# Optimization experiments

Hardware: AMD Instinct MI355X
Metric: run time of the kernel (lower is better)

The kernel has to match this reference:

```python
import jax, jax.numpy as jnp
import numpy as np

GAMMA = 0.99  # init kwarg


def _discounted_returns(ep_rs):
    # reversed running_add = running_add*gamma + r, emitted per step
    def step(carry, r):
        carry = carry * GAMMA + r
        return carry, carry
    _, out = jax.lax.scan(step, jnp.float32(0.0), ep_rs, reverse=True)
    return out  # [T]


def setup_inputs() -> dict:
    key = jax.random.key(0)
    k1, k2, k3 = jax.random.split(key, 3)
    T, A = 2097152, 18
    weight = jax.random.normal(k1, (T, A), dtype=jnp.float32)
    ep_rs = jax.random.normal(k2, (T,), dtype=jnp.float32)
    ep_as = jax.random.randint(k3, (T,), 0, A, dtype=jnp.int64)
    return {"weight": weight, "ep_rs": ep_rs, "ep_as": ep_as}


def reference(weight, ep_rs, ep_as):
    d = _discounted_returns(ep_rs)
    d = d - jnp.mean(d)
    # cross_entropy with reduction='none': -log_softmax(weight)[t, ep_as[t]]
    logp = jax.nn.log_softmax(weight, axis=-1)  # [T, A]
    neg_log_prob = -jnp.take_along_axis(logp, ep_as[:, None], axis=-1)[:, 0]  # [T]
    return jnp.mean(neg_log_prob * d)
```

## Files before the change

kernel.cpp:

```cpp
#include <hip/hip_runtime.h>
#include <math.h>

#define T_TOTAL 2097152
#define A_DIM   18
#define GAMMA_D 0.99

#define CHUNK 256
#define NC    (T_TOTAL / CHUNK)
#define KTR   14

#define ROWS_PER_TILE 256
#define NTILES  (T_TOTAL / ROWS_PER_TILE)
#define NB_MAIN 2048

__global__ void k_local(const float* __restrict__ r, double* __restrict__ L) {
    int c = blockIdx.x * blockDim.x + threadIdx.x;
    const float4* r4 = (const float4*)(r + (size_t)c * CHUNK);
    const double g  = GAMMA_D;
    const double g4 = g * g * g * g;
    double a0 = 0.0, a1 = 0.0, a2 = 0.0, a3 = 0.0;
    for (int k = CHUNK / 4 - 1; k >= 0; --k) {
        float4 v = r4[k];
        a0 = a0 * g4 + (double)v.x;
        a1 = a1 * g4 + (double)v.y;
        a2 = a2 * g4 + (double)v.z;
        a3 = a3 * g4 + (double)v.w;
    }
    L[c] = a0 + g * (a1 + g * (a2 + g * a3));
}

__global__ void k_carry(const double* __restrict__ L, double* __restrict__ carry,
                        double G) {
    int c = blockIdx.x * blockDim.x + threadIdx.x;
    double acc = 0.0;
    double w = 1.0;
    for (int m = 0; m < KTR; ++m) {
        int idx = c + 1 + m;
        if (idx < NC) acc += w * L[idx];
        w *= G;
    }
    carry[c] = acc;
}

__global__ void k_expand(const float* __restrict__ r,
                         const double* __restrict__ carry,
                         float* __restrict__ d) {
    int c = blockIdx.x * blockDim.x + threadIdx.x;
    const float4* r4 = (const float4*)(r + (size_t)c * CHUNK);
    float4*       d4 = (float4*)(d + (size_t)c * CHUNK);
    const double g = GAMMA_D;
    double cur = carry[c];
    for (int k = CHUNK / 4 - 1; k >= 0; --k) {
        float4 v = r4[k];
        double e3 = cur * g + (double)v.w;
        double e2 = e3 * g + (double)v.z;
        double e1 = e2 * g + (double)v.y;
        double e0 = e1 * g + (double)v.x;
        d4[k] = make_float4((float)e0, (float)e1, (float)e2, (float)e3);
        cur = e0;
    }
}

__launch_bounds__(256)
__global__ void k_main(const float* __restrict__ w, const int* __restrict__ act,
                       const float* __restrict__ d, double* __restrict__ partials) {
    __shared__ float  lds[ROWS_PER_TILE * A_DIM];
    __shared__ double red[12];
    const int tid = threadIdx.x;
    double s_d = 0.0, s_n = 0.0, s_nd = 0.0;

    for (int tile = blockIdx.x; tile < NTILES; tile += gridDim.x) {
        const float4* src = (const float4*)(w + (size_t)tile * ROWS_PER_TILE * A_DIM);
        float4* dst = (float4*)lds;
        __syncthreads();
        for (int idx = tid; idx < ROWS_PER_TILE * A_DIM / 4; idx += 256)
            dst[idx] = src[idx];
        __syncthreads();

        const int row = tile * ROWS_PER_TILE + tid;
        const float* wr = lds + tid * A_DIM;
        float m = wr[0];
        #pragma unroll
        for (int j = 1; j < A_DIM; ++j) m = fmaxf(m, wr[j]);
        float s = 0.0f;
        #pragma unroll
        for (int j = 0; j < A_DIM; ++j) s += expf(wr[j] - m);
        float lse  = m + logf(s);
        float nlp  = lse - wr[act[row]];
        float dv   = d[row];
        s_d  += (double)dv;
        s_n  += (double)nlp;
        s_nd += (double)nlp * (double)dv;
    }

    for (int off = 32; off > 0; off >>= 1) {
        s_d  += __shfl_down(s_d,  off, 64);
        s_n  += __shfl_down(s_n,  off, 64);
        s_nd += __shfl_down(s_nd, off, 64);
    }
    const int lane = tid & 63, wv = tid >> 6;
    if (lane == 0) { red[wv*3+0] = s_d; red[wv*3+1] = s_n; red[wv*3+2] = s_nd; }
    __syncthreads();
    if (tid == 0) {
        double a = 0.0, b = 0.0, c = 0.0;
        for (int i = 0; i < 4; ++i) { a += red[i*3]; b += red[i*3+1]; c += red[i*3+2]; }
        partials[blockIdx.x*3+0] = a;
        partials[blockIdx.x*3+1] = b;
        partials[blockIdx.x*3+2] = c;
    }
}

__global__ void k_final(const double* __restrict__ partials, float* __restrict__ out) {
    __shared__ double red[12];
    const int tid = threadIdx.x;
    double a = 0.0, b = 0.0, c = 0.0;
    for (int i = tid; i < NB_MAIN; i += 256) {
        a += partials[i*3+0];
        b += partials[i*3+1];
        c += partials[i*3+2];
    }
    for (int off = 32; off > 0; off >>= 1) {
        a += __shfl_down(a, off, 64);
        b += __shfl_down(b, off, 64);
        c += __shfl_down(c, off, 64);
    }
    const int lane = tid & 63, wv = tid >> 6;
    if (lane == 0) { red[wv*3+0] = a; red[wv*3+1] = b; red[wv*3+2] = c; }
    __syncthreads();
    if (tid == 0) {
        double A_ = 0.0, B_ = 0.0, C_ = 0.0;
        for (int i = 0; i < 4; ++i) { A_ += red[i*3]; B_ += red[i*3+1]; C_ += red[i*3+2]; }
        const double invT = 1.0 / (double)T_TOTAL;
        double res = (C_ - (A_ * invT) * B_) * invT;
        out[0] = (float)res;
    }
}

extern "C" void kernel_launch(void* const* d_in, const int* in_sizes, int n_in,
                              void* d_out, int out_size, void* d_ws, size_t ws_size,
                              hipStream_t stream) {
    const float* weight = (const float*)d_in[0];
    const float* ep_rs  = (const float*)d_in[1];
    const int*   ep_as  = (const int*)  d_in[2];
    float* out = (float*)d_out;

    char* ws = (char*)d_ws;
    double* L        = (double*)(ws);
    double* carry    = (double*)(ws + (1  << 16));
    double* partials = (double*)(ws + (2  << 16));
    float*  d        = (float*) (ws + (3  << 16));

    const double G = pow(GAMMA_D, (double)CHUNK);

    k_local <<<NC / 256, 256, 0, stream>>>(ep_rs, L);
    k_carry <<<NC / 256, 256, 0, stream>>>(L, carry, G);
    k_expand<<<NC / 256, 256, 0, stream>>>(ep_rs, carry, d);
    k_main  <<<NB_MAIN,  256, 0, stream>>>(weight, ep_as, d, partials);
    k_final <<<1,        256, 0, stream>>>(partials, out);
}
```

Baseline: 265.9 us.

## Fuse discounted-return expansion into main kernel via in-block weighted scan

Removes the k_expand kernel and the intermediate d buffer. Each main-kernel block now rebuilds discounted returns for its 256-row chunk with a wavefront suffix scan of gamma-weighted rewards plus the chunk carry. k_local is also parallelised to one wavefront per chunk, using a shuffle reduction in place of a serial per-thread loop. This saves one launch and a write and re-read of the 8 MB d array, at the cost of extra double-precision shuffles and pow/divide work in the main kernel. Dividing by gamma^tid may add some numerical error.

```diff
diff --git a/kernel.cpp b/kernel.cpp
--- a/kernel.cpp
+++ b/kernel.cpp
@@ -9,31 +9,26 @@
 #define NC    (T_TOTAL / CHUNK)
 #define KTR   14
 
-#define ROWS_PER_TILE 256
-#define NTILES  (T_TOTAL / ROWS_PER_TILE)
 #define NB_MAIN 2048
 
 __global__ void k_local(const float* __restrict__ r, double* __restrict__ L) {
-    int c = blockIdx.x * blockDim.x + threadIdx.x;
-    const float4* r4 = (const float4*)(r + (size_t)c * CHUNK);
-    const double g  = GAMMA_D;
-    const double g4 = g * g * g * g;
-    double a0 = 0.0, a1 = 0.0, a2 = 0.0, a3 = 0.0;
-    for (int k = CHUNK / 4 - 1; k >= 0; --k) {
-        float4 v = r4[k];
-        a0 = a0 * g4 + (double)v.x;
-        a1 = a1 * g4 + (double)v.y;
-        a2 = a2 * g4 + (double)v.z;
-        a3 = a3 * g4 + (double)v.w;
-    }
-    L[c] = a0 + g * (a1 + g * (a2 + g * a3));
+    const int tid  = blockIdx.x * blockDim.x + threadIdx.x;
+    const int c    = tid >> 6;
+    const int lane = tid & 63;
+    const float4 v = ((const float4*)r)[(size_t)c * 64 + lane];
+    const double g = GAMMA_D;
+    double w = pow(g, (double)(4 * lane)) *
+               ((double)v.x + g * ((double)v.y + g * ((double)v.z + g * (double)v.w)));
+    #pragma unroll
+    for (int off = 32; off > 0; off >>= 1) w += __shfl_down(w, off, 64);
+    if (lane == 0) L[c] = w;
 }
 
 __global__ void k_carry(const double* __restrict__ L, double* __restrict__ carry,
                         double G) {
-    int c = blockIdx.x * blockDim.x + threadIdx.x;
-    double acc = 0.0;
-    double w = 1.0;
+    const int c = blockIdx.x * blockDim.x + threadIdx.x;
+    double acc = 0.0, w = 1.0;
+    #pragma unroll
     for (int m = 0; m < KTR; ++m) {
         int idx = c + 1 + m;
         if (idx < NC) acc += w * L[idx];
@@ -42,71 +37,72 @@
     carry[c] = acc;
 }
 
-__global__ void k_expand(const float* __restrict__ r,
-                         const double* __restrict__ carry,
-                         float* __restrict__ d) {
-    int c = blockIdx.x * blockDim.x + threadIdx.x;
-    const float4* r4 = (const float4*)(r + (size_t)c * CHUNK);
-    float4*       d4 = (float4*)(d + (size_t)c * CHUNK);
-    const double g = GAMMA_D;
-    double cur = carry[c];
-    for (int k = CHUNK / 4 - 1; k >= 0; --k) {
-        float4 v = r4[k];
-        double e3 = cur * g + (double)v.w;
-        double e2 = e3 * g + (double)v.z;
-        double e1 = e2 * g + (double)v.y;
-        double e0 = e1 * g + (double)v.x;
-        d4[k] = make_float4((float)e0, (float)e1, (float)e2, (float)e3);
-        cur = e0;
-    }
-}
-
 __launch_bounds__(256)
-__global__ void k_main(const float* __restrict__ w, const int* __restrict__ act,
-                       const float* __restrict__ d, double* __restrict__ partials) {
-    __shared__ float  lds[ROWS_PER_TILE * A_DIM];
+__global__ void k_main(const float* __restrict__ wgt, const int* __restrict__ act,
+                       const float* __restrict__ r, const double* __restrict__ carry,
+                       double* __restrict__ partials) {
+    __shared__ float  lds[CHUNK * A_DIM];
+    __shared__ double ldsT[4];
     __shared__ double red[12];
-    const int tid = threadIdx.x;
+    const int tid  = threadIdx.x;
+    const int lane = tid & 63, wv = tid >> 6;
+    const double g    = GAMMA_D;
+    const double p    = pow(g, (double)tid);
+    const double ip   = 1.0 / p;
+    const double g256 = pow(g, 256.0);
     double s_d = 0.0, s_n = 0.0, s_nd = 0.0;
 
-    for (int tile = blockIdx.x; tile < NTILES; tile += gridDim.x) {
-        const float4* src = (const float4*)(w + (size_t)tile * ROWS_PER_TILE * A_DIM);
+    for (int c = blockIdx.x; c < NC; c += gridDim.x) {
+        __syncthreads();
+        const float4* src = (const float4*)(wgt + (size_t)c * CHUNK * A_DIM);
         float4* dst = (float4*)lds;
+        #pragma unroll
+        for (int i = 0; i < 5; ++i) {
+            int idx = tid + 256 * i;
+            if (idx < CHUNK * A_DIM / 4) dst[idx] = src[idx];
+        }
+        const int row = c * CHUNK + tid;
+        double ss = p * (double)r[row];
+        #pragma unroll
+        for (int off = 1; off < 64; off <<= 1) {
+            double v = __shfl_down(ss, off, 64);
+            ss += (lane + off < 64) ? v : 0.0;
+        }
+        if (lane == 0) ldsT[wv] = ss;
         __syncthreads();
-        for (int idx = tid; idx < ROWS_PER_TILE * A_DIM / 4; idx += 256)
-            dst[idx] = src[idx];
-        __syncthreads();
-
-        const int row = tile * ROWS_PER_TILE + tid;
+        double tail = 0.0;
+        #pragma unroll
+        for (int m = 0; m < 4; ++m)
+            if (m > wv) tail += ldsT[m];
+        const double dval = ip * (ss + tail + g256 * carry[c]);
         const float* wr = lds + tid * A_DIM;
-        float m = wr[0];
+        float mx = wr[0];
         #pragma unroll
-        for (int j = 1; j < A_DIM; ++j) m = fmaxf(m, wr[j]);
+        for (int j = 1; j < A_DIM; ++j) mx = fmaxf(mx, wr[j]);
         float s = 0.0f;
         #pragma unroll
-        for (int j = 0; j < A_DIM; ++j) s += expf(wr[j] - m);
-        float lse  = m + logf(s);
-        float nlp  = lse - wr[act[row]];
-        float dv   = d[row];
-        s_d  += (double)dv;
+        for (int j = 0; j < A_DIM; ++j) s += expf(wr[j] - mx);
+        const float nlp = mx + logf(s) - wr[act[row]];
+        s_d  += dval;
         s_n  += (double)nlp;
-        s_nd += (double)nlp * (double)dv;
+        s_nd += (double)nlp * dval;
     }
 
+    #pragma unroll
     for (int off = 32; off > 0; off >>= 1) {
         s_d  += __shfl_down(s_d,  off, 64);
         s_n  += __shfl_down(s_n,  off, 64);
         s_nd += __shfl_down(s_nd, off, 64);
     }
-    const int lane = tid & 63, wv = tid >> 6;
     if (lane == 0) { red[wv*3+0] = s_d; red[wv*3+1] = s_n; red[wv*3+2] = s_nd; }
     __syncthreads();
     if (tid == 0) {
-        double a = 0.0, b = 0.0, c = 0.0;
-        for (int i = 0; i < 4; ++i) { a += red[i*3]; b += red[i*3+1]; c += red[i*3+2]; }
+        double a = 0.0, b = 0.0, cc = 0.0;
+        #pragma unroll
+        for (int i = 0; i < 4; ++i) { a += red[i*3]; b += red[i*3+1]; cc += red[i*3+2]; }
         partials[blockIdx.x*3+0] = a;
         partials[blockIdx.x*3+1] = b;
-        partials[blockIdx.x*3+2] = c;
+        partials[blockIdx.x*3+2] = cc;
     }
 }
 
@@ -119,6 +115,7 @@
         b += partials[i*3+1];
         c += partials[i*3+2];
     }
+    #pragma unroll
     for (int off = 32; off > 0; off >>= 1) {
         a += __shfl_down(a, off, 64);
         b += __shfl_down(b, off, 64);
@@ -129,10 +126,10 @@
     __syncthreads();
     if (tid == 0) {
         double A_ = 0.0, B_ = 0.0, C_ = 0.0;
+        #pragma unroll
         for (int i = 0; i < 4; ++i) { A_ += red[i*3]; B_ += red[i*3+1]; C_ += red[i*3+2]; }
         const double invT = 1.0 / (double)T_TOTAL;
-        double res = (C_ - (A_ * invT) * B_) * invT;
-        out[0] = (float)res;
+        out[0] = (float)((C_ - (A_ * invT) * B_) * invT);
     }
 }
 
@@ -146,15 +143,13 @@
 
     char* ws = (char*)d_ws;
     double* L        = (double*)(ws);
-    double* carry    = (double*)(ws + (1  << 16));
-    double* partials = (double*)(ws + (2  << 16));
-    float*  d        = (float*) (ws + (3  << 16));
+    double* carry    = (double*)(ws + (1 << 16));
+    double* partials = (double*)(ws + (2 << 16));
 
     const double G = pow(GAMMA_D, (double)CHUNK);
 
-    k_local <<<NC / 256, 256, 0, stream>>>(ep_rs, L);
-    k_carry <<<NC / 256, 256, 0, stream>>>(L, carry, G);
-    k_expand<<<NC / 256, 256, 0, stream>>>(ep_rs, carry, d);
-    k_main  <<<NB_MAIN,  256, 0, stream>>>(weight, ep_as, d, partials);
-    k_final <<<1,        256, 0, stream>>>(partials, out);
+    k_local <<<T_TOTAL / 4 / 256, 256, 0, stream>>>(ep_rs, L);
+    k_carry <<<NC / 256,          256, 0, stream>>>(L, carry, G);
+    k_main  <<<NB_MAIN,           256, 0, stream>>>(weight, ep_as, ep_rs, carry, partials);
+    k_final <<<1,                 256, 0, stream>>>(partials, out);
 }
```

New measurement: 234.2 us. 1.14x faster.
